# Optimization experiments

Hardware: AMD Instinct MI355X
Metric: run time of the kernel (lower is better)

Reference implementation:

```python
import jax, jax.numpy as jnp
import numpy as np

V, D, C = 400000, 200, 45
B, S, KN, KC = 32, 128, 12, 10


def setup_inputs() -> dict:
    key = jax.random.key(0)
    k1, k2, k3, k4, k5, k6, k7 = jax.random.split(key, 7)
    return {
        "ngram_ids": jax.random.randint(k1, (B, S, KN), 0, V, dtype=jnp.int32),
        "ngram_mask": jax.random.randint(k2, (B, S, KN), 0, 2, dtype=jnp.int32),
        "ctx_ids": jax.random.randint(k3, (B, S, KC), 0, V, dtype=jnp.int32),
        "ctx_mask": jax.random.randint(k4, (B, S, KC), 0, 2, dtype=jnp.int32),
        # frozen pretrained embedding table (requires_grad=False in original)
        "embed": jax.random.normal(k5, (V, D), dtype=jnp.float32) * 0.1,
        # linear D*5 -> C (xavier-ish scale)
        "W": jax.random.normal(k6, (C, D * 5), dtype=jnp.float32) * (1.0 / np.sqrt(D * 5)),
        "b": jax.random.uniform(k7, (C,), dtype=jnp.float32,
                                 minval=-np.sqrt(6.0 / (D + 1)), maxval=np.sqrt(6.0 / (D + 1))),
    }


def _feat_context_embed(ngram_ids, ngram_mask, ctx_ids, ctx_mask, embed):
    # gather + masked sum over n-gram features and context features
    ng = embed[ngram_ids] * ngram_mask[..., None].astype(embed.dtype)   # [B,S,KN,D]
    cx = embed[ctx_ids] * ctx_mask[..., None].astype(embed.dtype)       # [B,S,KC,D]
    num = ng.sum(axis=2) + cx.sum(axis=2)                               # [B,S,D]
    cnt = (ngram_mask.sum(axis=-1) + ctx_mask.sum(axis=-1)).astype(embed.dtype)
    cnt = jnp.maximum(cnt, 1.0)  # original falls back to count=1 when no feature hits
    return num / cnt[..., None]


def _cat_window5(x):
    # zero-pad 2 words each side, concat 5-word window -> [B,S,5D]
    p = jnp.pad(x, ((0, 0), (2, 2), (0, 0)))
    s = x.shape[1]
    return jnp.concatenate([p[:, i:i + s] for i in range(5)], axis=-1)


def reference(ngram_ids, ngram_mask, ctx_ids, ctx_mask, embed, W, b):
    feat = _feat_context_embed(ngram_ids, ngram_mask, ctx_ids, ctx_mask, embed)  # [B,S,D]
    cated = _cat_window5(feat)                                                    # [B,S,5D]
    logit = jnp.einsum('bsf,cf->bsc', cated, W) + b                               # [B,S,C]
    return logit
```

## Files before the change

### kernel.cpp

```cpp
#include <hip/hip_runtime.h>
#include <hip/hip_bf16.h>

#define V  400000
#define D  200
#define DQ (D / 4)
#define C  45
#define B  32
#define S  128
#define KN 12
#define KC 10
#define KT (KN + KC)

#define STILE 16
#define NQ (STILE / 4)
#define CT 48
#define LT (STILE + 4)

__global__ __launch_bounds__(256) void feat_kernel(
    const int* __restrict__ ng_ids, const int* __restrict__ ng_mask,
    const int* __restrict__ cx_ids, const int* __restrict__ cx_mask,
    const float* __restrict__ embed, float* __restrict__ feat)
{
    const int lane = threadIdx.x & 63;
    const int row  = blockIdx.x * 4 + (threadIdx.x >> 6);

    int id = -1;
    if (lane < KN) {
        if (ng_mask[row * KN + lane]) id = ng_ids[row * KN + lane];
    } else if (lane < KT) {
        const int k = lane - KN;
        if (cx_mask[row * KC + k]) id = cx_ids[row * KC + k];
    }
    const unsigned long long bal = __ballot(id >= 0);
    const int cnt = __popcll(bal);
    const float inv = 1.0f / (float)(cnt > 0 ? cnt : 1);

    if (lane < DQ) {
        float4 acc0 = make_float4(0.f, 0.f, 0.f, 0.f);
        float4 acc1 = make_float4(0.f, 0.f, 0.f, 0.f);
        #pragma unroll
        for (int i = 0; i < KT; i += 2) {
            const int idA = __builtin_amdgcn_readlane(id, i);
            const int idB = __builtin_amdgcn_readlane(id, i + 1);
            float4 t0 = make_float4(0.f, 0.f, 0.f, 0.f);
            float4 t1 = make_float4(0.f, 0.f, 0.f, 0.f);
            if (idA >= 0)
                t0 = ((const float4*)(embed + (size_t)idA * D))[lane];
            if (idB >= 0)
                t1 = ((const float4*)(embed + (size_t)idB * D))[lane];
            acc0.x += t0.x; acc0.y += t0.y; acc0.z += t0.z; acc0.w += t0.w;
            acc1.x += t1.x; acc1.y += t1.y; acc1.z += t1.z; acc1.w += t1.w;
        }
        float4 r;
        r.x = (acc0.x + acc1.x) * inv;
        r.y = (acc0.y + acc1.y) * inv;
        r.z = (acc0.z + acc1.z) * inv;
        r.w = (acc0.w + acc1.w) * inv;
        ((float4*)(feat + (size_t)row * D))[lane] = r;
    }
}

__global__ __launch_bounds__(192) void logit_kernel(
    const float* __restrict__ feat, const float* __restrict__ W,
    const float* __restrict__ bias, float* __restrict__ out)
{
    const int b   = blockIdx.x >> 3;
    const int st  = (blockIdx.x & 7) * STILE;
    const int tid = threadIdx.x;

    __shared__ float4 lf[LT * DQ];

    const float4* feat4 = (const float4*)feat;
    for (int i = tid; i < LT * DQ; i += 192) {
        const int r  = i / DQ;
        const int dq = i - r * DQ;
        const int s  = st - 2 + r;
        float4 v = make_float4(0.f, 0.f, 0.f, 0.f);
        if (s >= 0 && s < S) v = feat4[(b * S + s) * DQ + dq];
        lf[i] = v;
    }
    __syncthreads();

    const int c = tid % CT;
    const int q = tid / CT;
    const bool cvalid = (c < C);
    const int cc = cvalid ? c : (C - 1);

    const float4* W4 = (const float4*)W;
    const float4* wbase = W4 + (size_t)cc * (5 * DQ);

    float acc[4] = {0.f, 0.f, 0.f, 0.f};

    for (int dq = 0; dq < DQ; ++dq) {
        float4 wv[5];
        #pragma unroll
        for (int w = 0; w < 5; ++w) wv[w] = wbase[w * DQ + dq];
        float4 fr[8];
        #pragma unroll
        for (int j = 0; j < 8; ++j) fr[j] = lf[(q * 4 + j) * DQ + dq];
        #pragma unroll
        for (int k = 0; k < 4; ++k) {
            #pragma unroll
            for (int w = 0; w < 5; ++w) {
                acc[k] += fr[k + w].x * wv[w].x + fr[k + w].y * wv[w].y
                        + fr[k + w].z * wv[w].z + fr[k + w].w * wv[w].w;
            }
        }
    }

    if (cvalid) {
        const float bv = bias[c];
        #pragma unroll
        for (int k = 0; k < 4; ++k) {
            const int s = st + q * 4 + k;
            out[((size_t)(b * S + s)) * C + c] = acc[k] + bv;
        }
    }
}

extern "C" void kernel_launch(void* const* d_in, const int* in_sizes, int n_in,
                              void* d_out, int out_size, void* d_ws, size_t ws_size,
                              hipStream_t stream)
{
    const int*   ng_ids  = (const int*)  d_in[0];
    const int*   ng_mask = (const int*)  d_in[1];
    const int*   cx_ids  = (const int*)  d_in[2];
    const int*   cx_mask = (const int*)  d_in[3];
    const float* embed   = (const float*)d_in[4];
    const float* W       = (const float*)d_in[5];
    const float* bias    = (const float*)d_in[6];
    float*       out     = (float*)d_out;

    float* feat = (float*)d_ws;

    feat_kernel<<<(B * S) / 4, 256, 0, stream>>>(ng_ids, ng_mask, cx_ids,
                                                 cx_mask, embed, feat);
    logit_kernel<<<B * (S / STILE), 192, 0, stream>>>(feat, W, bias, out);
}
```

Baseline: 422.7 us.

## Fuse embedding gather and windowed linear into one kernel with halo recompute

Replaces the two-kernel pipeline with one kernel. Each block gathers and averages the embedding rows for its 16-position tile plus a 4-row halo directly into shared memory, then runs the 5-word window linear layer from there. This removes the global round trip for the intermediate feature buffer and one kernel launch. Masked gathers become unconditional loads of row 0, zeroed by a multiply, so the loads can issue without branching. The cost is recomputing the halo rows (about 25% more gathers) and a much smaller grid: 256 blocks instead of 1024 feature blocks, which leaves fewer waves to hide the random-gather latency.

```diff
diff --git a/kernel.cpp b/kernel.cpp
--- a/kernel.cpp
+++ b/kernel.cpp
@@ -12,103 +12,97 @@
 #define KT (KN + KC)
 
 #define STILE 16
-#define NQ (STILE / 4)
-#define CT 48
 #define LT (STILE + 4)
+#define RPW (LT / 4)
 
-__global__ __launch_bounds__(256) void feat_kernel(
+__global__ __launch_bounds__(256) void fused_kernel(
     const int* __restrict__ ng_ids, const int* __restrict__ ng_mask,
     const int* __restrict__ cx_ids, const int* __restrict__ cx_mask,
-    const float* __restrict__ embed, float* __restrict__ feat)
-{
-    const int lane = threadIdx.x & 63;
-    const int row  = blockIdx.x * 4 + (threadIdx.x >> 6);
-
-    int id = -1;
-    if (lane < KN) {
-        if (ng_mask[row * KN + lane]) id = ng_ids[row * KN + lane];
-    } else if (lane < KT) {
-        const int k = lane - KN;
-        if (cx_mask[row * KC + k]) id = cx_ids[row * KC + k];
-    }
-    const unsigned long long bal = __ballot(id >= 0);
-    const int cnt = __popcll(bal);
-    const float inv = 1.0f / (float)(cnt > 0 ? cnt : 1);
-
-    if (lane < DQ) {
-        float4 acc0 = make_float4(0.f, 0.f, 0.f, 0.f);
-        float4 acc1 = make_float4(0.f, 0.f, 0.f, 0.f);
-        #pragma unroll
-        for (int i = 0; i < KT; i += 2) {
-            const int idA = __builtin_amdgcn_readlane(id, i);
-            const int idB = __builtin_amdgcn_readlane(id, i + 1);
-            float4 t0 = make_float4(0.f, 0.f, 0.f, 0.f);
-            float4 t1 = make_float4(0.f, 0.f, 0.f, 0.f);
-            if (idA >= 0)
-                t0 = ((const float4*)(embed + (size_t)idA * D))[lane];
-            if (idB >= 0)
-                t1 = ((const float4*)(embed + (size_t)idB * D))[lane];
-            acc0.x += t0.x; acc0.y += t0.y; acc0.z += t0.z; acc0.w += t0.w;
-            acc1.x += t1.x; acc1.y += t1.y; acc1.z += t1.z; acc1.w += t1.w;
-        }
-        float4 r;
-        r.x = (acc0.x + acc1.x) * inv;
-        r.y = (acc0.y + acc1.y) * inv;
-        r.z = (acc0.z + acc1.z) * inv;
-        r.w = (acc0.w + acc1.w) * inv;
-        ((float4*)(feat + (size_t)row * D))[lane] = r;
-    }
-}
-
-__global__ __launch_bounds__(192) void logit_kernel(
-    const float* __restrict__ feat, const float* __restrict__ W,
+    const float* __restrict__ embed, const float* __restrict__ W,
     const float* __restrict__ bias, float* __restrict__ out)
 {
-    const int b   = blockIdx.x >> 3;
-    const int st  = (blockIdx.x & 7) * STILE;
-    const int tid = threadIdx.x;
+    const int b    = blockIdx.x >> 3;
+    const int st   = (blockIdx.x & 7) * STILE;
+    const int tid  = threadIdx.x;
+    const int wave = tid >> 6;
+    const int lane = tid & 63;
 
     __shared__ float4 lf[LT * DQ];
 
-    const float4* feat4 = (const float4*)feat;
-    for (int i = tid; i < LT * DQ; i += 192) {
-        const int r  = i / DQ;
-        const int dq = i - r * DQ;
-        const int s  = st - 2 + r;
-        float4 v = make_float4(0.f, 0.f, 0.f, 0.f);
-        if (s >= 0 && s < S) v = feat4[(b * S + s) * DQ + dq];
-        lf[i] = v;
+    int                ids[RPW];
+    unsigned long long bal[RPW];
+    float              inv[RPW];
+    #pragma unroll
+    for (int r = 0; r < RPW; ++r) {
+        const int s = st - 2 + (wave * RPW + r);
+        int id = -1;
+        if (s >= 0 && s < S) {
+            const int row = b * S + s;
+            if (lane < KN) {
+                if (ng_mask[row * KN + lane]) id = ng_ids[row * KN + lane];
+            } else if (lane < KT) {
+                const int k = lane - KN;
+                if (cx_mask[row * KC + k]) id = cx_ids[row * KC + k];
+            }
+        }
+        bal[r] = __ballot(id >= 0);
+        ids[r] = (id >= 0) ? id : 0;
+        const int cnt = __popcll(bal[r]);
+        inv[r] = 1.0f / (float)(cnt > 0 ? cnt : 1);
+    }
+
+    if (lane < DQ) {
+        #pragma unroll
+        for (int r = 0; r < RPW; ++r) {
+            float4 a0 = make_float4(0.f, 0.f, 0.f, 0.f);
+            float4 a1 = make_float4(0.f, 0.f, 0.f, 0.f);
+            #pragma unroll
+            for (int i = 0; i < KT; i += 2) {
+                const int   iA = __builtin_amdgcn_readlane(ids[r], i);
+                const int   iB = __builtin_amdgcn_readlane(ids[r], i + 1);
+                const float wA = (float)((bal[r] >> i) & 1ULL);
+                const float wB = (float)((bal[r] >> (i + 1)) & 1ULL);
+                const float4 tA = ((const float4*)(embed + (size_t)iA * D))[lane];
+                const float4 tB = ((const float4*)(embed + (size_t)iB * D))[lane];
+                a0.x += tA.x * wA; a0.y += tA.y * wA;
+                a0.z += tA.z * wA; a0.w += tA.w * wA;
+                a1.x += tB.x * wB; a1.y += tB.y * wB;
+                a1.z += tB.z * wB; a1.w += tB.w * wB;
+            }
+            float4 rv;
+            rv.x = (a0.x + a1.x) * inv[r];
+            rv.y = (a0.y + a1.y) * inv[r];
+            rv.z = (a0.z + a1.z) * inv[r];
+            rv.w = (a0.w + a1.w) * inv[r];
+            lf[(wave * RPW + r) * DQ + lane] = rv;
+        }
     }
     __syncthreads();
 
-    const int c = tid % CT;
-    const int q = tid / CT;
-    const bool cvalid = (c < C);
-    const int cc = cvalid ? c : (C - 1);
+    const int c = lane;
+    const int q = wave;
+    if (c < C) {
+        const float4* wbase = (const float4*)W + (size_t)c * (5 * DQ);
+        float acc[4] = {0.f, 0.f, 0.f, 0.f};
 
-    const float4* W4 = (const float4*)W;
-    const float4* wbase = W4 + (size_t)cc * (5 * DQ);
-
-    float acc[4] = {0.f, 0.f, 0.f, 0.f};
-
-    for (int dq = 0; dq < DQ; ++dq) {
-        float4 wv[5];
-        #pragma unroll
-        for (int w = 0; w < 5; ++w) wv[w] = wbase[w * DQ + dq];
-        float4 fr[8];
-        #pragma unroll
-        for (int j = 0; j < 8; ++j) fr[j] = lf[(q * 4 + j) * DQ + dq];
-        #pragma unroll
-        for (int k = 0; k < 4; ++k) {
+        #pragma unroll 2
+        for (int dq = 0; dq < DQ; ++dq) {
+            float4 wv[5];
             #pragma unroll
-            for (int w = 0; w < 5; ++w) {
-                acc[k] += fr[k + w].x * wv[w].x + fr[k + w].y * wv[w].y
-                        + fr[k + w].z * wv[w].z + fr[k + w].w * wv[w].w;
+            for (int w = 0; w < 5; ++w) wv[w] = wbase[w * DQ + dq];
+            float4 fr[8];
+            #pragma unroll
+            for (int j = 0; j < 8; ++j) fr[j] = lf[(q * 4 + j) * DQ + dq];
+            #pragma unroll
+            for (int k = 0; k < 4; ++k) {
+                #pragma unroll
+                for (int w = 0; w < 5; ++w) {
+                    acc[k] += fr[k + w].x * wv[w].x + fr[k + w].y * wv[w].y
+                            + fr[k + w].z * wv[w].z + fr[k + w].w * wv[w].w;
+                }
             }
         }
-    }
 
-    if (cvalid) {
         const float bv = bias[c];
         #pragma unroll
         for (int k = 0; k < 4; ++k) {
@@ -131,9 +125,7 @@
     const float* bias    = (const float*)d_in[6];
     float*       out     = (float*)d_out;
 
-    float* feat = (float*)d_ws;
-
-    feat_kernel<<<(B * S) / 4, 256, 0, stream>>>(ng_ids, ng_mask, cx_ids,
-                                                 cx_mask, embed, feat);
-    logit_kernel<<<B * (S / STILE), 192, 0, stream>>>(feat, W, bias, out);
+    fused_kernel<<<B * (S / STILE), 256, 0, stream>>>(ng_ids, ng_mask, cx_ids,
+                                                      cx_mask, embed, W, bias,
+                                                      out);
 }
```

Result: faster. 409.6 us (-3.1%).
